# Kernel tuning notes

Hardware: AMD Instinct MI355X
Metric: run time of the kernel (lower is better)

The kernel has to match this reference:

```python
import jax, jax.numpy as jnp
import numpy as np

N_TOKENS = 16384
MODEL_DIM = 2048
NUM_EXPERTS = 64
K = 2


def setup_inputs() -> dict:
    key = jax.random.key(0)
    k1, k2 = jax.random.split(key)
    inputs = jax.random.normal(k1, (N_TOKENS, MODEL_DIM), dtype=jnp.float32)
    # gate weight, torch Linear(model_dim, num_experts, bias=False) -> [E, D]
    wg_weight = jax.random.normal(k2, (NUM_EXPERTS, MODEL_DIM), dtype=jnp.float32) * 0.02
    return {"inputs": inputs, "wg_weight": wg_weight}


def reference(inputs, wg_weight):
    E = wg_weight.shape[0]
    # gate computed in fp32 (module casts input and keeps wg in float32)
    logits = jnp.einsum("nd,ed->ne", inputs.astype(jnp.float32), wg_weight)
    probs = jax.nn.softmax(logits, axis=-1)                      # [N, E]
    topk_probs, topk_indices = jax.lax.top_k(probs, K)           # [N, K]
    flat_idx = topk_indices.reshape(-1)                          # [N*K]
    # stable sort of expert ids over all (token, slot) pairs
    sort_ordering = jnp.argsort(flat_idx)                        # [N*K]
    # reverse permutation: reversed[sort_ordering[i]] = i
    ar = jnp.arange(flat_idx.shape[0], dtype=sort_ordering.dtype)
    reversed_ordering = jnp.zeros_like(sort_ordering).at[sort_ordering].set(ar)
    # map slot index back to token index
    token_order = sort_ordering // K
    # per-expert counts (== unique_consecutive counts scattered into [E])
    input_splits = jnp.bincount(flat_idx, length=E).astype(jnp.int64)
    # combine weights: renormalize top-k probs via softmax when k > 1
    if K > 1:
        combine_weights = jax.nn.softmax(topk_probs, axis=-1)
    else:
        combine_weights = topk_probs
    combine_weights = combine_weights.reshape(-1).astype(inputs.dtype)
    return token_order, reversed_ordering, combine_weights, input_splits, probs
```

## Files before the change

kernel.cpp:

```cpp
#include <hip/hip_runtime.h>
#include <math.h>

#define N_TOKENS    16384
#define MODEL_DIM   2048
#define NUM_EXPERTS 64
#define NK          (N_TOKENS * 2)

#define OFF_TOKEN_ORDER 0
#define OFF_REVERSED    (NK)
#define OFF_COMBINE     (2 * NK)
#define OFF_SPLITS      (3 * NK)
#define OFF_PROBS       (3 * NK + NUM_EXPERTS)

#define NSEG 256
#define NFRAG 16384

typedef _Float16 half8 __attribute__((ext_vector_type(8)));
typedef float    f32x4 __attribute__((ext_vector_type(4)));
typedef double   d64x2 __attribute__((ext_vector_type(2)));

__global__ __launch_bounds__(256) void preconvert(
    const float* __restrict__ w, half8* __restrict__ WH, half8* __restrict__ WL,
    int* __restrict__ segHist)
{
    const int fr = blockIdx.x * 256 + threadIdx.x;
    const int lane = fr & 63;
    const int tile = (fr >> 6) & 3;
    const int kstep = fr >> 8;
    const int e = tile * 16 + (lane & 15);
    const int kb = kstep * 32 + (lane >> 4) * 8;
    const float* src = w + (size_t)e * MODEL_DIM + kb;
    const float4 w0 = *(const float4*)(src);
    const float4 w1 = *(const float4*)(src + 4);
    const float av[8] = {w0.x, w0.y, w0.z, w0.w, w1.x, w1.y, w1.z, w1.w};
    half8 hh, hl;
#pragma unroll
    for (int j = 0; j < 8; j++) {
        const float v = av[j] * 64.0f;
        const _Float16 h = (_Float16)v;
        hh[j] = h;
        hl[j] = (_Float16)((v - (float)h) * 4096.0f);
    }
    WH[fr] = hh;
    WL[fr] = hl;
    segHist[fr] = 0;
}

template<int NS>
__global__ __launch_bounds__(256) void gate_partial(
    const float* __restrict__ x, const half8* __restrict__ WH,
    const half8* __restrict__ WL, double* __restrict__ part, int S)
{
    const int tid  = threadIdx.x;
    const int wv   = tid >> 6;
    const int lane = tid & 63;
    const int tb   = blockIdx.x;
    const int sp   = blockIdx.y;
    const int col  = lane & 15;
    const int kg   = lane >> 4;

    const float* pA = x + (size_t)(tb * 64 + wv * 16 + col) * MODEL_DIM
                    + (size_t)sp * NS * 32 + kg * 8;
    const size_t fb = (size_t)sp * NS * 4 * 64 + lane;
    const half8* pbh = WH + fb;
    const half8* pbl = WL + fb;

    f32x4 accH[4], accC[4];
    double accD[4][4];
#pragma unroll
    for (int t = 0; t < 4; t++) {
        accH[t] = (f32x4){0.f, 0.f, 0.f, 0.f};
        accC[t] = (f32x4){0.f, 0.f, 0.f, 0.f};
#pragma unroll
        for (int r = 0; r < 4; r++) accD[t][r] = 0.0;
    }

#pragma unroll
    for (int j = 0; j < NS; j++) {
        const float4 a0 = *(const float4*)(pA + j * 32);
        const float4 a1 = *(const float4*)(pA + j * 32 + 4);
        const float av[8] = {a0.x, a0.y, a0.z, a0.w, a1.x, a1.y, a1.z, a1.w};
        half8 ah, al;
#pragma unroll
        for (int q = 0; q < 8; q++) {
            const float v = av[q];
            const _Float16 h = (_Float16)v;
            ah[q] = h;
            al[q] = (_Float16)((v - (float)h) * 4096.0f);
        }
#pragma unroll
        for (int t = 0; t < 4; t++) {
            const half8 bh = pbh[(j * 4 + t) * 64];
            const half8 bl = pbl[(j * 4 + t) * 64];
            accH[t] = __builtin_amdgcn_mfma_f32_16x16x32_f16(ah, bh, accH[t], 0, 0, 0);
            accC[t] = __builtin_amdgcn_mfma_f32_16x16x32_f16(ah, bl, accC[t], 0, 0, 0);
            accC[t] = __builtin_amdgcn_mfma_f32_16x16x32_f16(al, bh, accC[t], 0, 0, 0);
        }
        if ((j & 7) == 7) {
#pragma unroll
            for (int t = 0; t < 4; t++)
#pragma unroll
                for (int r = 0; r < 4; r++) {
                    accD[t][r] += (double)accH[t][r] + (double)accC[t][r] * (1.0 / 4096.0);
                    accH[t][r] = 0.0f;
                    accC[t][r] = 0.0f;
                }
        }
    }

    double* dst = part + ((size_t)(tb * 4 + wv) * S + sp) * 1024 + (size_t)lane * 4;
#pragma unroll
    for (int t = 0; t < 4; t++) {
        *(d64x2*)(dst + t * 256)     = (d64x2){accD[t][0], accD[t][1]};
        *(d64x2*)(dst + t * 256 + 2) = (d64x2){accD[t][2], accD[t][3]};
    }
}

__global__ __launch_bounds__(256) void reduce_kernel(
    const double* __restrict__ part, float* __restrict__ out,
    int* __restrict__ flat_idx, int* __restrict__ segHist, int S)
{
    const int tid  = threadIdx.x;
    const int wv   = tid >> 6;
    const int lane = tid & 63;
    const int tb   = blockIdx.x;
    const int t0   = tb * 64;
    const int col  = lane & 15;

    const double* src = part + ((size_t)(tb * 4 + wv) * S) * 1024 + (size_t)lane * 4;

    double accD[4][4];
#pragma unroll
    for (int t = 0; t < 4; t++)
#pragma unroll
        for (int r = 0; r < 4; r++) accD[t][r] = 0.0;

    for (int sp = 0; sp < S; sp++) {
#pragma unroll
        for (int t = 0; t < 4; t++) {
            const d64x2 v0 = *(const d64x2*)(src + (size_t)sp * 1024 + t * 256);
            const d64x2 v1 = *(const d64x2*)(src + (size_t)sp * 1024 + t * 256 + 2);
            accD[t][0] += v0[0]; accD[t][1] += v0[1];
            accD[t][2] += v1[0]; accD[t][3] += v1[1];
        }
    }

    const int rowg = lane >> 4;
#pragma unroll
    for (int r = 0; r < 4; r++) {
        float lv[4];
#pragma unroll
        for (int t = 0; t < 4; t++) lv[t] = (float)(accD[t][r] * (1.0 / 64.0));

        float m = fmaxf(fmaxf(lv[0], lv[1]), fmaxf(lv[2], lv[3]));
#pragma unroll
        for (int d = 1; d < 16; d <<= 1) m = fmaxf(m, __shfl_xor(m, d));

        float l1 = -INFINITY, l2 = -INFINITY;
        int i1 = 0, i2 = 0;
#pragma unroll
        for (int t = 0; t < 4; t++) {
            const float l = lv[t];
            const int e = t * 16 + col;
            if (l > l1)      { l2 = l1; i2 = i1; l1 = l; i1 = e; }
            else if (l > l2) { l2 = l;  i2 = e; }
        }
#pragma unroll
        for (int d = 1; d < 16; d <<= 1) {
            const float ol1 = __shfl_xor(l1, d), ol2 = __shfl_xor(l2, d);
            const int   oi1 = __shfl_xor(i1, d), oi2 = __shfl_xor(i2, d);
            if (ol1 > l1 || (ol1 == l1 && oi1 < i1)) {
                if (l1 > ol2 || (l1 == ol2 && i1 < oi2)) { l2 = l1;  i2 = i1;  }
                else                                     { l2 = ol2; i2 = oi2; }
                l1 = ol1; i1 = oi1;
            } else if (ol1 > l2 || (ol1 == l2 && oi1 < i2)) {
                l2 = ol1; i2 = oi1;
            }
        }

        float ex[4];
        double sd = 0.0;
#pragma unroll
        for (int t = 0; t < 4; t++) { ex[t] = expf(lv[t] - m); sd += (double)ex[t]; }
#pragma unroll
        for (int d = 1; d < 16; d <<= 1) sd += __shfl_xor(sd, d);
        const float inv = (float)(1.0 / sd);

        const int tok = t0 + wv * 16 + rowg * 4 + r;
        float* pp2 = out + OFF_PROBS + (size_t)tok * NUM_EXPERTS + col;
#pragma unroll
        for (int t = 0; t < 4; t++) pp2[t * 16] = ex[t] * inv;

        if (col == 0) {
            const float p1 = expf(l1 - m) * inv;
            const float p2 = expf(l2 - m) * inv;
            const float e2 = expf(p2 - p1);
            const float rr2 = 1.0f / (1.0f + e2);
            out[OFF_COMBINE + 2 * tok]     = rr2;
            out[OFF_COMBINE + 2 * tok + 1] = e2 * rr2;
            flat_idx[2 * tok]     = i1;
            flat_idx[2 * tok + 1] = i2;
            atomicAdd(&segHist[(tok >> 6) * NUM_EXPERTS + i1], 1);
            atomicAdd(&segHist[(tok >> 6) * NUM_EXPERTS + i2], 1);
        }
    }
}

__global__ __launch_bounds__(256) void scan_scatter(
    const int* __restrict__ flat_idx, const int* __restrict__ segHist,
    float* __restrict__ out)
{
    __shared__ int h[NSEG * NUM_EXPERTS];
    __shared__ int gtot[4 * NUM_EXPERTS];
    __shared__ int base_[NUM_EXPERTS];
    __shared__ int cnt[2 * NUM_EXPERTS];

    const int tid = threadIdx.x;
    for (int i = tid; i < NSEG * NUM_EXPERTS / 4; i += 256)
        *(int4*)(h + i * 4) = *(const int4*)(segHist + i * 4);
    if (tid < 2 * NUM_EXPERTS) cnt[tid] = 0;
    __syncthreads();

    const int e = tid & 63;
    const int g = tid >> 6;
    int run = 0;
    for (int s = g * 64; s < g * 64 + 64; s++) {
        const int idx = s * NUM_EXPERTS + e;
        const int v = h[idx];
        h[idx] = run;
        run += v;
    }
    gtot[g * NUM_EXPERTS + e] = run;
    __syncthreads();

    if (tid < NUM_EXPERTS) {
        int b = 0;
#pragma unroll
        for (int gg = 0; gg < 4; gg++) {
            const int t = gtot[gg * NUM_EXPERTS + tid];
            gtot[gg * NUM_EXPERTS + tid] = b;
            b += t;
        }
        if (blockIdx.x == 0) out[OFF_SPLITS + tid] = (float)b;
        int xs = b;
#pragma unroll
        for (int off = 1; off < 64; off <<= 1) {
            const int v = __shfl_up(xs, off);
            if (tid >= off) xs += v;
        }
        base_[tid] = xs - b;
    }
    __syncthreads();

    const int i = blockIdx.x * 256 + tid;
    const int ee = flat_idx[i];
    const int lane = tid & 63;
    const int wv = tid >> 6;
    const int segslot = wv >> 1;
    const int seg = i >> 7;

    unsigned long long match = ~0ull;
#pragma unroll
    for (int b = 0; b < 6; b++) {
        const unsigned long long m = __ballot((ee >> b) & 1);
        match &= ((ee >> b) & 1) ? m : ~m;
    }
    const int rank = __popcll(match & ((1ull << lane) - 1ull));

    const int segoff = h[seg * NUM_EXPERTS + ee]
                     + gtot[(seg >> 6) * NUM_EXPERTS + ee] + base_[ee];

    int pos = 0;
    if ((wv & 1) == 0) {
        pos = segoff + rank;
        if (lane == __builtin_ctzll(match))
            cnt[segslot * NUM_EXPERTS + ee] = __popcll(match);
    }
    __syncthreads();
    if ((wv & 1) == 1)
        pos = segoff + cnt[segslot * NUM_EXPERTS + ee] + rank;

    out[OFF_TOKEN_ORDER + pos] = (float)(i >> 1);
    out[OFF_REVERSED + i]      = (float)pos;
}

extern "C" void kernel_launch(void* const* d_in, const int* in_sizes, int n_in,
                              void* d_out, int out_size, void* d_ws, size_t ws_size,
                              hipStream_t stream) {
    const float* x = (const float*)d_in[0];
    const float* w = (const float*)d_in[1];
    float* out = (float*)d_out;

    int* flat_idx = (int*)d_ws;
    int* segHist  = flat_idx + NK;
    half8* WH = (half8*)(segHist + NSEG * NUM_EXPERTS);
    half8* WL = WH + NFRAG;
    double* part = (double*)(WL + NFRAG);

    const size_t fixed_bytes = (size_t)NK * 4 + NSEG * NUM_EXPERTS * 4
                             + 2 * (size_t)NFRAG * 16;
    const size_t avail = ws_size > fixed_bytes ? ws_size - fixed_bytes : 0;
    const size_t per = (size_t)N_TOKENS * NUM_EXPERTS * 8;

    int S;
    if      (avail >= 8 * per) S = 8;
    else if (avail >= 4 * per) S = 4;
    else if (avail >= 2 * per) S = 2;
    else                       S = 1;

    preconvert<<<64, 256, 0, stream>>>(w, WH, WL, segHist);
    switch (S) {
        case 8: gate_partial<8> <<<dim3(256, 8), 256, 0, stream>>>(x, WH, WL, part, 8); break;
        case 4: gate_partial<16><<<dim3(256, 4), 256, 0, stream>>>(x, WH, WL, part, 4); break;
        case 2: gate_partial<32><<<dim3(256, 2), 256, 0, stream>>>(x, WH, WL, part, 2); break;
        default: gate_partial<64><<<dim3(256, 1), 256, 0, stream>>>(x, WH, WL, part, 1); break;
    }
    reduce_kernel<<<256, 256, 0, stream>>>(part, out, flat_idx, segHist, S);
    scan_scatter<<<NK / 256, 256, 0, stream>>>(flat_idx, segHist, out);
}
```

Measured before the change: 243.9 us.

## Fuse weight split into gate GEMM and process two row tiles per wave

Drops the separate preconvert kernel and has each wave load the fp32 gate weights and split them into hi/lo fp16 inline. Each wave now computes two 16-row token tiles, so each converted weight fragment feeds twice as many MFMAs and the grid is halved. segHist zeroing moves into the gate kernel, and occupancy is pinned to two waves per EU. This removes one launch and the weight staging buffer, but adds per-block conversion arithmetic and strided fp32 weight loads, and raises register pressure.

After: 243.1 us. Within noise of the previous version (-0.3%).

```diff
diff --git a/kernel.cpp b/kernel.cpp
--- a/kernel.cpp
+++ b/kernel.cpp
@@ -13,43 +13,28 @@
 #define OFF_PROBS       (3 * NK + NUM_EXPERTS)
 
 #define NSEG 256
-#define NFRAG 16384
 
 typedef _Float16 half8 __attribute__((ext_vector_type(8)));
 typedef float    f32x4 __attribute__((ext_vector_type(4)));
 typedef double   d64x2 __attribute__((ext_vector_type(2)));
 
-__global__ __launch_bounds__(256) void preconvert(
-    const float* __restrict__ w, half8* __restrict__ WH, half8* __restrict__ WL,
-    int* __restrict__ segHist)
-{
-    const int fr = blockIdx.x * 256 + threadIdx.x;
-    const int lane = fr & 63;
-    const int tile = (fr >> 6) & 3;
-    const int kstep = fr >> 8;
-    const int e = tile * 16 + (lane & 15);
-    const int kb = kstep * 32 + (lane >> 4) * 8;
-    const float* src = w + (size_t)e * MODEL_DIM + kb;
-    const float4 w0 = *(const float4*)(src);
-    const float4 w1 = *(const float4*)(src + 4);
-    const float av[8] = {w0.x, w0.y, w0.z, w0.w, w1.x, w1.y, w1.z, w1.w};
-    half8 hh, hl;
-#pragma unroll
-    for (int j = 0; j < 8; j++) {
-        const float v = av[j] * 64.0f;
+__device__ __forceinline__ void fsplit(const float4 a, const float4 b, const float s,
+                                       half8& hh, half8& hl) {
+    const float av[8] = {a.x, a.y, a.z, a.w, b.x, b.y, b.z, b.w};
+#pragma unroll
+    for (int q = 0; q < 8; q++) {
+        const float v = av[q] * s;
         const _Float16 h = (_Float16)v;
-        hh[j] = h;
-        hl[j] = (_Float16)((v - (float)h) * 4096.0f);
-    }
-    WH[fr] = hh;
-    WL[fr] = hl;
-    segHist[fr] = 0;
+        hh[q] = h;
+        hl[q] = (_Float16)((v - (float)h) * 4096.0f);
+    }
 }
 
 template<int NS>
-__global__ __launch_bounds__(256) void gate_partial(
-    const float* __restrict__ x, const half8* __restrict__ WH,
-    const half8* __restrict__ WL, double* __restrict__ part, int S)
+__global__ __attribute__((amdgpu_waves_per_eu(2, 2))) __launch_bounds__(256)
+void gate_partial(
+    const float* __restrict__ x, const float* __restrict__ w,
+    double* __restrict__ part, int S, int* __restrict__ segHist)
 {
     const int tid  = threadIdx.x;
     const int wv   = tid >> 6;
@@ -59,60 +44,73 @@
     const int col  = lane & 15;
     const int kg   = lane >> 4;
 
-    const float* pA = x + (size_t)(tb * 64 + wv * 16 + col) * MODEL_DIM
-                    + (size_t)sp * NS * 32 + kg * 8;
-    const size_t fb = (size_t)sp * NS * 4 * 64 + lane;
-    const half8* pbh = WH + fb;
-    const half8* pbl = WL + fb;
-
-    f32x4 accH[4], accC[4];
-    double accD[4][4];
-#pragma unroll
-    for (int t = 0; t < 4; t++) {
-        accH[t] = (f32x4){0.f, 0.f, 0.f, 0.f};
-        accC[t] = (f32x4){0.f, 0.f, 0.f, 0.f};
-#pragma unroll
-        for (int r = 0; r < 4; r++) accD[t][r] = 0.0;
-    }
+    if (sp == 0 && tid < 128) segHist[tb * 128 + tid] = 0;
+
+    const int kbase = sp * NS * 32 + kg * 8;
+    const float* pA0 = x + (size_t)(tb * 128 + wv * 32 + col) * MODEL_DIM + kbase;
+    const float* pA1 = pA0 + (size_t)16 * MODEL_DIM;
+    const float* pB  = w + (size_t)col * MODEL_DIM + kbase;
+
+    f32x4 accH[2][4], accC[2][4];
+    double accD[2][4][4];
+#pragma unroll
+    for (int tt = 0; tt < 2; tt++)
+#pragma unroll
+        for (int t = 0; t < 4; t++) {
+            accH[tt][t] = (f32x4){0.f, 0.f, 0.f, 0.f};
+            accC[tt][t] = (f32x4){0.f, 0.f, 0.f, 0.f};
+#pragma unroll
+            for (int r = 0; r < 4; r++) accD[tt][t][r] = 0.0;
+        }
 
 #pragma unroll
     for (int j = 0; j < NS; j++) {
-        const float4 a0 = *(const float4*)(pA + j * 32);
-        const float4 a1 = *(const float4*)(pA + j * 32 + 4);
-        const float av[8] = {a0.x, a0.y, a0.z, a0.w, a1.x, a1.y, a1.z, a1.w};
-        half8 ah, al;
-#pragma unroll
-        for (int q = 0; q < 8; q++) {
-            const float v = av[q];
-            const _Float16 h = (_Float16)v;
-            ah[q] = h;
-            al[q] = (_Float16)((v - (float)h) * 4096.0f);
-        }
+        const float4 a00 = *(const float4*)(pA0 + j * 32);
+        const float4 a01 = *(const float4*)(pA0 + j * 32 + 4);
+        const float4 a10 = *(const float4*)(pA1 + j * 32);
+        const float4 a11 = *(const float4*)(pA1 + j * 32 + 4);
+        half8 ah[2], al[2];
+        fsplit(a00, a01, 1.0f, ah[0], al[0]);
+        fsplit(a10, a11, 1.0f, ah[1], al[1]);
+
+#pragma unroll
+        for (int kt = 0; kt < 4; kt++) {
+            const float4 b0 = *(const float4*)(pB + (size_t)kt * 16 * MODEL_DIM + j * 32);
+            const float4 b1 = *(const float4*)(pB + (size_t)kt * 16 * MODEL_DIM + j * 32 + 4);
+            half8 bh, bl;
+            fsplit(b0, b1, 64.0f, bh, bl);
+#pragma unroll
+            for (int tt = 0; tt < 2; tt++) {
+                accH[tt][kt] = __builtin_amdgcn_mfma_f32_16x16x32_f16(ah[tt], bh, accH[tt][kt], 0, 0, 0);
+                accC[tt][kt] = __builtin_amdgcn_mfma_f32_16x16x32_f16(ah[tt], bl, accC[tt][kt], 0, 0, 0);
+                accC[tt][kt] = __builtin_amdgcn_mfma_f32_16x16x32_f16(al[tt], bh, accC[tt][kt], 0, 0, 0);
+            }
+        }
+
+        if ((j & 7) == 7) {
+#pragma unroll
+            for (int tt = 0; tt < 2; tt++)
+#pragma unroll
+                for (int t = 0; t < 4; t++)
+#pragma unroll
+                    for (int r = 0; r < 4; r++) {
+                        accD[tt][t][r] += (double)accH[tt][t][r]
+                                        + (double)accC[tt][t][r] * (1.0 / 4096.0);
+                        accH[tt][t][r] = 0.0f;
+                        accC[tt][t][r] = 0.0f;
+                    }
+        }
+    }
+
+#pragma unroll
+    for (int tt = 0; tt < 2; tt++) {
+        const int tile = tb * 8 + wv * 2 + tt;
+        double* dst = part + ((size_t)tile * S + sp) * 1024 + (size_t)lane * 4;
 #pragma unroll
         for (int t = 0; t < 4; t++) {
-            const half8 bh = pbh[(j * 4 + t) * 64];
-            const half8 bl = pbl[(j * 4 + t) * 64];
-            accH[t] = __builtin_amdgcn_mfma_f32_16x16x32_f16(ah, bh, accH[t], 0, 0, 0);
-            accC[t] = __builtin_amdgcn_mfma_f32_16x16x32_f16(ah, bl, accC[t], 0, 0, 0);
-            accC[t] = __builtin_amdgcn_mfma_f32_16x16x32_f16(al, bh, accC[t], 0, 0, 0);
-        }
-        if ((j & 7) == 7) {
-#pragma unroll
-            for (int t = 0; t < 4; t++)
-#pragma unroll
-                for (int r = 0; r < 4; r++) {
-                    accD[t][r] += (double)accH[t][r] + (double)accC[t][r] * (1.0 / 4096.0);
-                    accH[t][r] = 0.0f;
-                    accC[t][r] = 0.0f;
-                }
-        }
-    }
-
-    double* dst = part + ((size_t)(tb * 4 + wv) * S + sp) * 1024 + (size_t)lane * 4;
-#pragma unroll
-    for (int t = 0; t < 4; t++) {
-        *(d64x2*)(dst + t * 256)     = (d64x2){accD[t][0], accD[t][1]};
-        *(d64x2*)(dst + t * 256 + 2) = (d64x2){accD[t][2], accD[t][3]};
+            *(d64x2*)(dst + t * 256)     = (d64x2){accD[tt][t][0], accD[tt][t][1]};
+            *(d64x2*)(dst + t * 256 + 2) = (d64x2){accD[tt][t][2], accD[tt][t][3]};
+        }
     }
 }
 
@@ -293,12 +291,9 @@
 
     int* flat_idx = (int*)d_ws;
     int* segHist  = flat_idx + NK;
-    half8* WH = (half8*)(segHist + NSEG * NUM_EXPERTS);
-    half8* WL = WH + NFRAG;
-    double* part = (double*)(WL + NFRAG);
-
-    const size_t fixed_bytes = (size_t)NK * 4 + NSEG * NUM_EXPERTS * 4
-                             + 2 * (size_t)NFRAG * 16;
+    double* part  = (double*)(segHist + NSEG * NUM_EXPERTS);
+
+    const size_t fixed_bytes = (size_t)NK * 4 + NSEG * NUM_EXPERTS * 4;
     const size_t avail = ws_size > fixed_bytes ? ws_size - fixed_bytes : 0;
     const size_t per = (size_t)N_TOKENS * NUM_EXPERTS * 8;
 
@@ -308,12 +303,11 @@
     else if (avail >= 2 * per) S = 2;
     else                       S = 1;
 
-    preconvert<<<64, 256, 0, stream>>>(w, WH, WL, segHist);
     switch (S) {
-        case 8: gate_partial<8> <<<dim3(256, 8), 256, 0, stream>>>(x, WH, WL, part, 8); break;
-        case 4: gate_partial<16><<<dim3(256, 4), 256, 0, stream>>>(x, WH, WL, part, 4); break;
-        case 2: gate_partial<32><<<dim3(256, 2), 256, 0, stream>>>(x, WH, WL, part, 2); break;
-        default: gate_partial<64><<<dim3(256, 1), 256, 0, stream>>>(x, WH, WL, part, 1); break;
+        case 8: gate_partial<8> <<<dim3(128, 8), 256, 0, stream>>>(x, w, part, 8, segHist); break;
+        case 4: gate_partial<16><<<dim3(128, 4), 256, 0, stream>>>(x, w, part, 4, segHist); break;
+        case 2: gate_partial<32><<<dim3(128, 2), 256, 0, stream>>>(x, w, part, 2, segHist); break;
+        default: gate_partial<64><<<dim3(128, 1), 256, 0, stream>>>(x, w, part, 1, segHist); break;
     }
     reduce_kernel<<<256, 256, 0, stream>>>(part, out, flat_idx, segHist, S);
     scan_scatter<<<NK / 256, 256, 0, stream>>>(flat_idx, segHist, out);
```
